# Performance work log

Measured on AMD Instinct MI355X. Metric: run time of the kernel, lower is better.

The kernel has to match this reference:

```python
import jax, jax.numpy as jnp
import numpy as np

BINS = jnp.array([1, 2, 3, 4, 8, 16, 32, 64], dtype=jnp.int32)
L = 10      # max span width
HID = 150   # Score hidden dim


def _mlp(x, W1, b1, W2, b2, W3, b3):
    # Score module: Linear -> ReLU -> Linear -> ReLU -> Linear (dropout = identity at eval)
    h = jax.nn.relu(x @ W1 + b1)
    h = jax.nn.relu(h @ W2 + b2)
    return h @ W3 + b3


def setup_inputs() -> dict:
    key = jax.random.key(0)
    ks = jax.random.split(key, 16)
    T, A, E, D, S = 8192, 1024, 512, 20, 32768
    GI = 2 * A + E + D  # 2580
    sc = lambda n: 1.0 / np.sqrt(n)
    return {
        "states": jax.random.normal(ks[0], (T, A), jnp.float32),
        "embeds": jax.random.normal(ks[1], (T, E), jnp.float32),
        "span_starts": jnp.sort(jax.random.randint(ks[2], (S,), 0, T - L)),
        "span_lengths": jax.random.randint(ks[3], (S,), 0, L),
        # attention Score params (attn_dim -> 150 -> 150 -> 1)
        "Wa1": jax.random.normal(ks[4], (A, HID), jnp.float32) * sc(A),
        "ba1": jnp.zeros((HID,), jnp.float32),
        "Wa2": jax.random.normal(ks[5], (HID, HID), jnp.float32) * sc(HID),
        "ba2": jnp.zeros((HID,), jnp.float32),
        "Wa3": jax.random.normal(ks[6], (HID, 1), jnp.float32) * sc(HID),
        "ba3": jnp.zeros((1,), jnp.float32),
        # Distance embedding table (len(bins)+1 = 9 buckets)
        "width_table": jax.random.normal(ks[7], (9, D), jnp.float32) * 0.1,
        # mention Score params (gi_dim -> 150 -> 150 -> 1)
        "Ws1": jax.random.normal(ks[8], (GI, HID), jnp.float32) * sc(GI),
        "bs1": jnp.zeros((HID,), jnp.float32),
        "Ws2": jax.random.normal(ks[9], (HID, HID), jnp.float32) * sc(HID),
        "bs2": jnp.zeros((HID,), jnp.float32),
        "Ws3": jax.random.normal(ks[10], (HID, 1), jnp.float32) * sc(HID),
        "bs3": jnp.zeros((1,), jnp.float32),
    }


def reference(states, embeds, span_starts, span_lengths,
              Wa1, ba1, Wa2, ba2, Wa3, ba3,
              width_table,
              Ws1, bs1, Ws2, bs2, Ws3, bs3):
    T = states.shape[0]
    # per-token attention logits: [T, 1]
    attns = _mlp(states, Wa1, ba1, Wa2, ba2, Wa3, ba3)

    pos = jnp.arange(L)
    idx = span_starts[:, None] + pos[None, :]                 # [S, L]
    mask = pos[None, :] <= span_lengths[:, None]              # valid positions
    idx = jnp.minimum(idx, T - 1)

    span_attn = jnp.where(mask, attns[idx, 0], -jnp.inf)      # [S, L]
    w = jax.nn.softmax(span_attn, axis=1)                     # per-span softmax
    pooled = jnp.einsum('sl,sle->se', w, embeds[idx])         # [S, E]

    ends = span_starts + span_lengths
    widths = span_lengths + 1
    bucket = jnp.searchsorted(BINS, widths.astype(jnp.int32), side='right')
    size_emb = width_table[bucket]                            # [S, D]

    g = jnp.concatenate([states[span_starts], states[ends], pooled, size_emb], axis=-1)
    scores = _mlp(g, Ws1, bs1, Ws2, bs2, Ws3, bs3)[:, 0]      # [S]
    return scores
```

## Files before the change

### kernel.cpp

```cpp
#include <hip/hip_runtime.h>
#include <math.h>

#define T_TOK 8192
#define A_DIM 1024
#define E_DIM 512
#define S_SPAN 32768
#define HID 150

typedef __attribute__((ext_vector_type(8))) short short8;
typedef __attribute__((ext_vector_type(4))) float f32x4;
typedef __attribute__((ext_vector_type(4))) unsigned int u32x4;

__device__ __forceinline__ unsigned short f2bf(float f) {
    unsigned int u = __builtin_bit_cast(unsigned int, f);
    u += 0x7FFFu + ((u >> 16) & 1u);
    return (unsigned short)(u >> 16);
}
__device__ __forceinline__ float bf2f(unsigned int h16) {
    unsigned int u = h16 << 16;
    return __builtin_bit_cast(float, u);
}
__device__ __forceinline__ short8 cast8(f32x4 a, f32x4 b) {
    short8 r;
    r[0] = (short)f2bf(a.x); r[1] = (short)f2bf(a.y);
    r[2] = (short)f2bf(a.z); r[3] = (short)f2bf(a.w);
    r[4] = (short)f2bf(b.x); r[5] = (short)f2bf(b.y);
    r[6] = (short)f2bf(b.z); r[7] = (short)f2bf(b.w);
    return r;
}

__device__ __forceinline__ void pub_barrier() {
    __builtin_amdgcn_sched_barrier(0);
    asm volatile("s_waitcnt lgkmcnt(0)" ::: "memory");
    __builtin_amdgcn_sched_barrier(0);
    __builtin_amdgcn_s_barrier();
    __builtin_amdgcn_sched_barrier(0);
}

struct WConv { const float* src; unsigned short* dst; int K0; int Kpad; int nblk; };
struct PrepTab {
    WConv g[6];
    const float* wt; const float* Ws1w; const float* bs1; float* PW;
};

__global__ __launch_bounds__(256) void prep_kernel(PrepTab tab) {
    __shared__ float tl[64][65];
    int b = blockIdx.x;
    #pragma unroll
    for (int gi = 0; gi < 6; ++gi) {
        if (b < tab.g[gi].nblk) {
            const int kt   = tab.g[gi].Kpad >> 6;
            const int j0   = (b / kt) * 64;
            const int k0   = (b % kt) * 64;
            const int K0   = tab.g[gi].K0;
            const int Kpad = tab.g[gi].Kpad;
            const int ty = threadIdx.x >> 6, tx = threadIdx.x & 63;
            const float* src = tab.g[gi].src;
            #pragma unroll
            for (int r = 0; r < 16; ++r) {
                int k = k0 + ty * 16 + r;
                int j = j0 + tx;
                tl[ty * 16 + r][tx] = (j < HID && k < K0)
                                      ? src[(size_t)k * HID + j] : 0.f;
            }
            __syncthreads();
            unsigned short* dst = tab.g[gi].dst;
            #pragma unroll
            for (int r = 0; r < 16; ++r) {
                int j = j0 + ty * 16 + r;
                if (j < 160)
                    dst[(size_t)j * Kpad + k0 + tx] = f2bf(tl[tx][ty * 16 + r]);
            }
            return;
        }
        b -= tab.g[gi].nblk;
    }
    int j = threadIdx.x;
    if (j < 160) {
        float acc = 0.f;
        if (j < HID) {
            for (int k = 0; k < 20; ++k)
                acc = fmaf(tab.wt[b * 20 + k], tab.Ws1w[k * HID + j], acc);
            acc += tab.bs1[j];
        }
        tab.PW[b * 160 + j] = acc;
    }
}

struct GG {
    const void* A; int lda;
    const unsigned short* W; int K; int nrb;
    unsigned short* outh; int ldo;
    const float* bias; int relu;
    const float* dotv; const float* dotb; float* dotout;
    const unsigned short* W2; const float* bias2;
};
struct GTab { GG g[4]; int ng; };

template <int TAG, bool AF32>
__global__ __launch_bounds__(256) void gemm_fused(GTab tab) {
    constexpr int LDW = 72;
    __shared__ unsigned short WtL[2][160 * LDW];

    int b = blockIdx.x;
    int gi = 0;
    while (gi < tab.ng - 1 && b >= tab.g[gi].nrb) { b -= tab.g[gi].nrb; ++gi; }
    const GG G = tab.g[gi];

    const int tid = threadIdx.x;
    const int wid = tid >> 6;
    const int lane = tid & 63;
    const int l15 = lane & 15;
    const int quad = lane >> 4;
    const int row0 = b * 64 + wid * 16 + l15;
    const int K = G.K;
    const int nch = K >> 6;
    const float* Af = (const float*)G.A + (size_t)row0 * G.lda;
    const unsigned short* Ah = (const unsigned short*)G.A + (size_t)row0 * G.lda;

    int sn[5], sk[5];
    #pragma unroll
    for (int i = 0; i < 5; ++i) { int u = tid + i * 256; sn[i] = u >> 3; sk[i] = (u & 7) * 8; }

    f32x4 acc[10];
    #pragma unroll
    for (int nt = 0; nt < 10; ++nt) acc[nt] = (f32x4){0.f, 0.f, 0.f, 0.f};

    u32x4 wA[5], wB[5];
    f32x4 fAa[4], fAb[4];
    short8 hAa[2], hAb[2];
    short8 avc0, avc1;

#define LOAD_W(SET, KOFF)                                                     \
    {   _Pragma("unroll")                                                     \
        for (int i = 0; i < 5; ++i)                                           \
            SET[i] = *(const u32x4*)(G.W + (size_t)sn[i] * K + (KOFF) + sk[i]); }
#define LOAD_A(FSET, HSET, KOFF)                                              \
    if (AF32) {                                                               \
        FSET[0] = *(const f32x4*)(Af + (KOFF) + quad * 8);                    \
        FSET[1] = *(const f32x4*)(Af + (KOFF) + quad * 8 + 4);                \
        FSET[2] = *(const f32x4*)(Af + (KOFF) + 32 + quad * 8);               \
        FSET[3] = *(const f32x4*)(Af + (KOFF) + 32 + quad * 8 + 4);           \
    } else {                                                                  \
        HSET[0] = *(const short8*)(Ah + (KOFF) + quad * 8);                   \
        HSET[1] = *(const short8*)(Ah + (KOFF) + 32 + quad * 8);              \
    }
#define STORE_W(SET, BUF)                                                     \
    {   _Pragma("unroll")                                                     \
        for (int i = 0; i < 5; ++i)                                           \
            *(u32x4*)&WtL[BUF][sn[i] * LDW + sk[i]] = SET[i]; }
#define SET_AVC(FSET, HSET)                                                   \
    if (AF32) { avc0 = cast8(FSET[0], FSET[1]); avc1 = cast8(FSET[2], FSET[3]); } \
    else      { avc0 = HSET[0]; avc1 = HSET[1]; }
#define MFMA_BLOCK(BUF)                                                       \
    {   _Pragma("unroll")                                                     \
        for (int nt = 0; nt < 10; ++nt) {                                     \
            short8 bv0 = *(const short8*)&WtL[BUF][(nt * 16 + l15) * LDW + quad * 8]; \
            acc[nt] = __builtin_amdgcn_mfma_f32_16x16x32_bf16(avc0, bv0, acc[nt], 0, 0, 0); \
            short8 bv1 = *(const short8*)&WtL[BUF][(nt * 16 + l15) * LDW + 32 + quad * 8]; \
            acc[nt] = __builtin_amdgcn_mfma_f32_16x16x32_bf16(avc1, bv1, acc[nt], 0, 0, 0); \
        } }

    LOAD_W(wA, 0);
    LOAD_A(fAa, hAa, 0);
    LOAD_W(wB, 64);
    LOAD_A(fAb, hAb, 64);
    STORE_W(wA, 0);
    SET_AVC(fAa, hAa);
    pub_barrier();

    for (int c = 0; c + 1 < nch; c += 2) {
        const bool mA = (c + 2 < nch);
        if (mA) {
            const int kn = (c + 2) << 6;
            LOAD_W(wA, kn);
            LOAD_A(fAa, hAa, kn);
        }
        STORE_W(wB, 1);
        MFMA_BLOCK(0);
        SET_AVC(fAb, hAb);
        pub_barrier();

        const bool mB = (c + 3 < nch);
        if (mB) {
            const int kn = (c + 3) << 6;
            LOAD_W(wB, kn);
            LOAD_A(fAb, hAb, kn);
        }
        if (mA) STORE_W(wA, 0);
        MFMA_BLOCK(1);
        if (mA) SET_AVC(fAa, hAa);
        pub_barrier();
    }
    if (nch & 1) {
        MFMA_BLOCK(0);
    }

#undef LOAD_W
#undef LOAD_A
#undef STORE_W
#undef SET_AVC
#undef MFMA_BLOCK

    const int rbase = b * 64 + wid * 16 + quad * 4;
    if (G.W2) {
        constexpr int LDH = 168;
        unsigned short* tile = &WtL[0][0] + wid * 16 * LDH;
        #pragma unroll
        for (int nt = 0; nt < 10; ++nt) {
            int col = nt * 16 + l15;
            float bv_ = (col < HID) ? G.bias[col] : 0.f;
            #pragma unroll
            for (int r = 0; r < 4; ++r) {
                float v = fmaxf(acc[nt][r] + bv_, 0.f);
                tile[(quad * 4 + r) * LDH + col] = f2bf(v);
            }
        }
        f32x4 acc2[10];
        #pragma unroll
        for (int nt = 0; nt < 10; ++nt) acc2[nt] = (f32x4){0.f, 0.f, 0.f, 0.f};
        #pragma unroll
        for (int kc = 0; kc < 5; ++kc) {
            short8 av = *(const short8*)&tile[l15 * LDH + kc * 32 + quad * 8];
            #pragma unroll
            for (int nt = 0; nt < 10; ++nt) {
                short8 bv = *(const short8*)(G.W2 + (size_t)(nt * 16 + l15) * 192 + kc * 32 + quad * 8);
                acc2[nt] = __builtin_amdgcn_mfma_f32_16x16x32_bf16(av, bv, acc2[nt], 0, 0, 0);
            }
        }
        float part[4] = {0.f, 0.f, 0.f, 0.f};
        #pragma unroll
        for (int nt = 0; nt < 10; ++nt) {
            int col = nt * 16 + l15;
            float b2 = (col < HID) ? G.bias2[col] : 0.f;
            float vv = (col < HID) ? G.dotv[col] : 0.f;
            #pragma unroll
            for (int r = 0; r < 4; ++r)
                part[r] += fmaxf(acc2[nt][r] + b2, 0.f) * vv;
        }
        #pragma unroll
        for (int r = 0; r < 4; ++r) {
            float p = part[r];
            #pragma unroll
            for (int off = 1; off < 16; off <<= 1) p += __shfl_xor(p, off);
            if (l15 == 0) G.dotout[rbase + r] = p + G.dotb[0];
        }
    } else if (G.dotout) {
        float part[4] = {0.f, 0.f, 0.f, 0.f};
        #pragma unroll
        for (int nt = 0; nt < 10; ++nt) {
            int col = nt * 16 + l15;
            float bv_ = (col < HID) ? G.bias[col] : 0.f;
            float vv = (col < HID) ? G.dotv[col] : 0.f;
            #pragma unroll
            for (int r = 0; r < 4; ++r)
                part[r] += fmaxf(acc[nt][r] + bv_, 0.f) * vv;
        }
        #pragma unroll
        for (int r = 0; r < 4; ++r) {
            float p = part[r];
            #pragma unroll
            for (int off = 1; off < 16; off <<= 1) p += __shfl_xor(p, off);
            if (l15 == 0) G.dotout[rbase + r] = p + G.dotb[0];
        }
    } else {
        #pragma unroll
        for (int nt = 0; nt < 10; ++nt) {
            int col = nt * 16 + l15;
            float bv_ = (G.bias != nullptr && col < HID) ? G.bias[col] : 0.f;
            #pragma unroll
            for (int r = 0; r < 4; ++r) {
                int row = rbase + r;
                float v = acc[nt][r] + bv_;
                if (G.relu) v = fmaxf(v, 0.f);
                G.outh[(size_t)row * G.ldo + col] = f2bf(v);
            }
        }
    }
}

__global__ __launch_bounds__(256) void span_l1_kernel(const float* __restrict__ attns,
                                                      const int* __restrict__ starts,
                                                      const int* __restrict__ lens,
                                                      const unsigned short* __restrict__ Ps,
                                                      const unsigned short* __restrict__ Pe,
                                                      const unsigned short* __restrict__ Pm,
                                                      const float* __restrict__ PW,
                                                      unsigned short* __restrict__ SH1) {
    const int wid = threadIdx.x >> 6;
    const int lane = threadIdx.x & 63;
    const int grp = lane >> 4;
    const int hl = lane & 15;
    const int gbase = lane & 48;
    const int s = blockIdx.x * 16 + wid * 4 + grp;
    const int start = starts[s];
    const int len = lens[s];

    const int iv = min(start + hl, T_TOK - 1);
    float a = (hl <= len) ? attns[iv] : -INFINITY;
    float m = a;
    #pragma unroll
    for (int off = 8; off; off >>= 1) m = fmaxf(m, __shfl_xor(m, off));
    float e = (hl <= len) ? __expf(a - m) : 0.f;
    float ssum = e;
    #pragma unroll
    for (int off = 8; off; off >>= 1) ssum += __shfl_xor(ssum, off);
    float wv = e / ssum;

    float wl[10]; int il[10];
    #pragma unroll
    for (int l = 0; l < 10; ++l) {
        wl[l] = __shfl(wv, gbase + l);
        il[l] = __shfl(iv, gbase + l);
    }

    const int end = start + len;
    const int width = len + 1;
    const int bucket = (width >= 1) + (width >= 2) + (width >= 3) + (width >= 4) +
                       (width >= 8) + (width >= 16) + (width >= 32) + (width >= 64);

    const unsigned short* ps = Ps + (size_t)start * 160;
    const unsigned short* pe = Pe + (size_t)end * 160;
    const float* pw = PW + bucket * 160;

    for (int p = hl; p < 75; p += 16) {
        const int j = 2 * p;
        unsigned int u0 = *(const unsigned int*)(ps + j);
        unsigned int u1 = *(const unsigned int*)(pe + j);
        float a0 = pw[j]     + bf2f(u0 & 0xffff) + bf2f(u1 & 0xffff);
        float a1 = pw[j + 1] + bf2f(u0 >> 16)    + bf2f(u1 >> 16);
        #pragma unroll
        for (int l = 0; l < 10; ++l) {
            unsigned int um = *(const unsigned int*)(Pm + (size_t)il[l] * 160 + j);
            a0 = fmaf(wl[l], bf2f(um & 0xffff), a0);
            a1 = fmaf(wl[l], bf2f(um >> 16), a1);
        }
        unsigned int packed = (unsigned int)f2bf(fmaxf(a0, 0.f)) |
                              ((unsigned int)f2bf(fmaxf(a1, 0.f)) << 16);
        *(unsigned int*)(SH1 + (size_t)s * 192 + j) = packed;
    }
}

extern "C" void kernel_launch(void* const* d_in, const int* in_sizes, int n_in,
                              void* d_out, int out_size, void* d_ws, size_t ws_size,
                              hipStream_t stream) {
    const float* states = (const float*)d_in[0];
    const float* embeds = (const float*)d_in[1];
    const int* span_starts = (const int*)d_in[2];
    const int* span_lengths = (const int*)d_in[3];
    const float* Wa1 = (const float*)d_in[4];
    const float* ba1 = (const float*)d_in[5];
    const float* Wa2 = (const float*)d_in[6];
    const float* ba2 = (const float*)d_in[7];
    const float* Wa3 = (const float*)d_in[8];
    const float* ba3 = (const float*)d_in[9];
    const float* width_table = (const float*)d_in[10];
    const float* Ws1 = (const float*)d_in[11];
    const float* bs1 = (const float*)d_in[12];
    const float* Ws2 = (const float*)d_in[13];
    const float* bs2 = (const float*)d_in[14];
    const float* Ws3 = (const float*)d_in[15];
    const float* bs3 = (const float*)d_in[16];
    float* out = (float*)d_out;

    char* w = (char*)d_ws;
    unsigned short* WtA  = (unsigned short*)w;  w += 480 * 1024 * 2;
    unsigned short* WtE  = (unsigned short*)w;  w += 160 * 512 * 2;
    unsigned short* Wa2t = (unsigned short*)w;  w += 160 * 192 * 2;
    unsigned short* Ws2t = (unsigned short*)w;  w += 160 * 192 * 2;
    float* PW    = (float*)w;                   w += 9 * 160 * 4;
    float* attns = (float*)w;                   w += 8192 * 4;
    unsigned short* Psh = (unsigned short*)w;   w += (size_t)T_TOK * 160 * 2;
    unsigned short* Peh = (unsigned short*)w;   w += (size_t)T_TOK * 160 * 2;
    unsigned short* Pmh = (unsigned short*)w;   w += (size_t)T_TOK * 160 * 2;
    unsigned short* SH1 = (unsigned short*)w;   w += (size_t)S_SPAN * 192 * 2;

    PrepTab pt;
    pt.g[0] = { Wa1,              WtA,              1024, 1024, 3 * (1024/64) };
    pt.g[1] = { Ws1,              WtA + 160*1024,   1024, 1024, 3 * (1024/64) };
    pt.g[2] = { Ws1 + 1024*150,   WtA + 320*1024,   1024, 1024, 3 * (1024/64) };
    pt.g[3] = { Ws1 + 2048*150,   WtE,               512,  512, 3 * (512/64)  };
    pt.g[4] = { Wa2,              Wa2t,              150,  192, 3 * (192/64)  };
    pt.g[5] = { Ws2,              Ws2t,              150,  192, 3 * (192/64)  };
    pt.wt = width_table; pt.Ws1w = Ws1 + 2560*150; pt.bs1 = bs1; pt.PW = PW;
    int wblk = 0; for (int i = 0; i < 6; ++i) wblk += pt.g[i].nblk;
    prep_kernel<<<wblk + 9, 256, 0, stream>>>(pt);

    GG z = {};

    GTab t1; t1.ng = 4;
    t1.g[0] = z; t1.g[0].A = states; t1.g[0].lda = 1024; t1.g[0].W = WtA;            t1.g[0].K = 1024;
    t1.g[0].nrb = 128; t1.g[0].bias = ba1;
    t1.g[0].W2 = Wa2t; t1.g[0].bias2 = ba2;
    t1.g[0].dotv = Wa3; t1.g[0].dotb = ba3; t1.g[0].dotout = attns;
    t1.g[1] = z; t1.g[1].A = states; t1.g[1].lda = 1024; t1.g[1].W = WtA + 160*1024; t1.g[1].K = 1024;
    t1.g[1].nrb = 128; t1.g[1].outh = Psh; t1.g[1].ldo = 160;
    t1.g[2] = z; t1.g[2].A = states; t1.g[2].lda = 1024; t1.g[2].W = WtA + 320*1024; t1.g[2].K = 1024;
    t1.g[2].nrb = 128; t1.g[2].outh = Peh; t1.g[2].ldo = 160;
    t1.g[3] = z; t1.g[3].A = embeds; t1.g[3].lda = 512;  t1.g[3].W = WtE;            t1.g[3].K = 512;
    t1.g[3].nrb = 128; t1.g[3].outh = Pmh; t1.g[3].ldo = 160;
    gemm_fused<1, true><<<512, 256, 0, stream>>>(t1);

    span_l1_kernel<<<S_SPAN / 16, 256, 0, stream>>>(attns, span_starts, span_lengths,
                                                    Psh, Peh, Pmh, PW, SH1);

    GTab t3; t3.ng = 1;
    t3.g[0] = z; t3.g[0].A = SH1; t3.g[0].lda = 192; t3.g[0].W = Ws2t; t3.g[0].K = 192;
    t3.g[0].nrb = 512; t3.g[0].bias = bs2; t3.g[0].dotv = Ws3; t3.g[0].dotb = bs3; t3.g[0].dotout = out;
    gemm_fused<3, false><<<512, 256, 0, stream>>>(t3);
}
```

Measured before the change: 166.0 us.

## Read GEMM weights directly from global memory and vectorize span layer-1 gathers

The fused GEMM drops its double-buffered LDS staging of weight tiles and its barriers. Each wave now loads bf16 weight fragments straight from global/L2 for every MFMA, and LDS is kept only for the per-wave epilogue tile. Separately, the span layer-1 kernel switches from 4-byte to 16-byte vector loads and stores, with each lane handling 8 hidden columns and the gathered row offsets premultiplied. This removes LDS traffic and synchronisation, but every wave now redundantly refetches the same weight tile from cache and loses the prefetch overlap.

```diff
diff --git a/kernel.cpp b/kernel.cpp
--- a/kernel.cpp
+++ b/kernel.cpp
@@ -27,14 +27,6 @@
     r[4] = (short)f2bf(b.x); r[5] = (short)f2bf(b.y);
     r[6] = (short)f2bf(b.z); r[7] = (short)f2bf(b.w);
     return r;
-}
-
-__device__ __forceinline__ void pub_barrier() {
-    __builtin_amdgcn_sched_barrier(0);
-    asm volatile("s_waitcnt lgkmcnt(0)" ::: "memory");
-    __builtin_amdgcn_sched_barrier(0);
-    __builtin_amdgcn_s_barrier();
-    __builtin_amdgcn_sched_barrier(0);
 }
 
 struct WConv { const float* src; unsigned short* dst; int K0; int Kpad; int nblk; };
@@ -99,8 +91,8 @@
 
 template <int TAG, bool AF32>
 __global__ __launch_bounds__(256) void gemm_fused(GTab tab) {
-    constexpr int LDW = 72;
-    __shared__ unsigned short WtL[2][160 * LDW];
+    constexpr int LDH = 168;
+    __shared__ unsigned short tileAll[4][16 * LDH];
 
     int b = blockIdx.x;
     int gi = 0;
@@ -117,95 +109,38 @@
     const int nch = K >> 6;
     const float* Af = (const float*)G.A + (size_t)row0 * G.lda;
     const unsigned short* Ah = (const unsigned short*)G.A + (size_t)row0 * G.lda;
-
-    int sn[5], sk[5];
-    #pragma unroll
-    for (int i = 0; i < 5; ++i) { int u = tid + i * 256; sn[i] = u >> 3; sk[i] = (u & 7) * 8; }
+    const unsigned short* Wr = G.W + (size_t)l15 * K;
 
     f32x4 acc[10];
     #pragma unroll
     for (int nt = 0; nt < 10; ++nt) acc[nt] = (f32x4){0.f, 0.f, 0.f, 0.f};
 
-    u32x4 wA[5], wB[5];
-    f32x4 fAa[4], fAb[4];
-    short8 hAa[2], hAb[2];
-    short8 avc0, avc1;
-
-#define LOAD_W(SET, KOFF)                                                     \
-    {   _Pragma("unroll")                                                     \
-        for (int i = 0; i < 5; ++i)                                           \
-            SET[i] = *(const u32x4*)(G.W + (size_t)sn[i] * K + (KOFF) + sk[i]); }
-#define LOAD_A(FSET, HSET, KOFF)                                              \
-    if (AF32) {                                                               \
-        FSET[0] = *(const f32x4*)(Af + (KOFF) + quad * 8);                    \
-        FSET[1] = *(const f32x4*)(Af + (KOFF) + quad * 8 + 4);                \
-        FSET[2] = *(const f32x4*)(Af + (KOFF) + 32 + quad * 8);               \
-        FSET[3] = *(const f32x4*)(Af + (KOFF) + 32 + quad * 8 + 4);           \
-    } else {                                                                  \
-        HSET[0] = *(const short8*)(Ah + (KOFF) + quad * 8);                   \
-        HSET[1] = *(const short8*)(Ah + (KOFF) + 32 + quad * 8);              \
-    }
-#define STORE_W(SET, BUF)                                                     \
-    {   _Pragma("unroll")                                                     \
-        for (int i = 0; i < 5; ++i)                                           \
-            *(u32x4*)&WtL[BUF][sn[i] * LDW + sk[i]] = SET[i]; }
-#define SET_AVC(FSET, HSET)                                                   \
-    if (AF32) { avc0 = cast8(FSET[0], FSET[1]); avc1 = cast8(FSET[2], FSET[3]); } \
-    else      { avc0 = HSET[0]; avc1 = HSET[1]; }
-#define MFMA_BLOCK(BUF)                                                       \
-    {   _Pragma("unroll")                                                     \
-        for (int nt = 0; nt < 10; ++nt) {                                     \
-            short8 bv0 = *(const short8*)&WtL[BUF][(nt * 16 + l15) * LDW + quad * 8]; \
-            acc[nt] = __builtin_amdgcn_mfma_f32_16x16x32_bf16(avc0, bv0, acc[nt], 0, 0, 0); \
-            short8 bv1 = *(const short8*)&WtL[BUF][(nt * 16 + l15) * LDW + 32 + quad * 8]; \
-            acc[nt] = __builtin_amdgcn_mfma_f32_16x16x32_bf16(avc1, bv1, acc[nt], 0, 0, 0); \
-        } }
-
-    LOAD_W(wA, 0);
-    LOAD_A(fAa, hAa, 0);
-    LOAD_W(wB, 64);
-    LOAD_A(fAb, hAb, 64);
-    STORE_W(wA, 0);
-    SET_AVC(fAa, hAa);
-    pub_barrier();
-
-    for (int c = 0; c + 1 < nch; c += 2) {
-        const bool mA = (c + 2 < nch);
-        if (mA) {
-            const int kn = (c + 2) << 6;
-            LOAD_W(wA, kn);
-            LOAD_A(fAa, hAa, kn);
-        }
-        STORE_W(wB, 1);
-        MFMA_BLOCK(0);
-        SET_AVC(fAb, hAb);
-        pub_barrier();
-
-        const bool mB = (c + 3 < nch);
-        if (mB) {
-            const int kn = (c + 3) << 6;
-            LOAD_W(wB, kn);
-            LOAD_A(fAb, hAb, kn);
-        }
-        if (mA) STORE_W(wA, 0);
-        MFMA_BLOCK(1);
-        if (mA) SET_AVC(fAa, hAa);
-        pub_barrier();
-    }
-    if (nch & 1) {
-        MFMA_BLOCK(0);
-    }
-
-#undef LOAD_W
-#undef LOAD_A
-#undef STORE_W
-#undef SET_AVC
-#undef MFMA_BLOCK
+    for (int c = 0; c < nch; ++c) {
+        const int kb = c << 6;
+        short8 avc0, avc1;
+        if (AF32) {
+            f32x4 f0 = *(const f32x4*)(Af + kb + quad * 8);
+            f32x4 f1 = *(const f32x4*)(Af + kb + quad * 8 + 4);
+            f32x4 f2 = *(const f32x4*)(Af + kb + 32 + quad * 8);
+            f32x4 f3 = *(const f32x4*)(Af + kb + 32 + quad * 8 + 4);
+            avc0 = cast8(f0, f1);
+            avc1 = cast8(f2, f3);
+        } else {
+            avc0 = *(const short8*)(Ah + kb + quad * 8);
+            avc1 = *(const short8*)(Ah + kb + 32 + quad * 8);
+        }
+        #pragma unroll
+        for (int nt = 0; nt < 10; ++nt) {
+            short8 bv0 = *(const short8*)(Wr + (size_t)nt * 16 * K + kb + quad * 8);
+            acc[nt] = __builtin_amdgcn_mfma_f32_16x16x32_bf16(avc0, bv0, acc[nt], 0, 0, 0);
+            short8 bv1 = *(const short8*)(Wr + (size_t)nt * 16 * K + kb + 32 + quad * 8);
+            acc[nt] = __builtin_amdgcn_mfma_f32_16x16x32_bf16(avc1, bv1, acc[nt], 0, 0, 0);
+        }
+    }
 
     const int rbase = b * 64 + wid * 16 + quad * 4;
     if (G.W2) {
-        constexpr int LDH = 168;
-        unsigned short* tile = &WtL[0][0] + wid * 16 * LDH;
+        unsigned short* tile = tileAll[wid];
         #pragma unroll
         for (int nt = 0; nt < 10; ++nt) {
             int col = nt * 16 + l15;
@@ -277,6 +212,19 @@
             }
         }
     }
+}
+
+__device__ __forceinline__ void add_bf8(f32x4& A, f32x4& B, u32x4 u) {
+    A.x += bf2f(u.x & 0xffff); A.y += bf2f(u.x >> 16);
+    A.z += bf2f(u.y & 0xffff); A.w += bf2f(u.y >> 16);
+    B.x += bf2f(u.z & 0xffff); B.y += bf2f(u.z >> 16);
+    B.z += bf2f(u.w & 0xffff); B.w += bf2f(u.w >> 16);
+}
+__device__ __forceinline__ void fma_bf8(f32x4& A, f32x4& B, u32x4 u, float w) {
+    A.x = fmaf(w, bf2f(u.x & 0xffff), A.x); A.y = fmaf(w, bf2f(u.x >> 16), A.y);
+    A.z = fmaf(w, bf2f(u.y & 0xffff), A.z); A.w = fmaf(w, bf2f(u.y >> 16), A.w);
+    B.x = fmaf(w, bf2f(u.z & 0xffff), B.x); B.y = fmaf(w, bf2f(u.z >> 16), B.y);
+    B.z = fmaf(w, bf2f(u.w & 0xffff), B.z); B.w = fmaf(w, bf2f(u.w >> 16), B.w);
 }
 
 __global__ __launch_bounds__(256) void span_l1_kernel(const float* __restrict__ attns,
@@ -311,7 +259,7 @@
     #pragma unroll
     for (int l = 0; l < 10; ++l) {
         wl[l] = __shfl(wv, gbase + l);
-        il[l] = __shfl(iv, gbase + l);
+        il[l] = __shfl(iv, gbase + l) * 160;
     }
 
     const int end = start + len;
@@ -323,21 +271,25 @@
     const unsigned short* pe = Pe + (size_t)end * 160;
     const float* pw = PW + bucket * 160;
 
-    for (int p = hl; p < 75; p += 16) {
-        const int j = 2 * p;
-        unsigned int u0 = *(const unsigned int*)(ps + j);
-        unsigned int u1 = *(const unsigned int*)(pe + j);
-        float a0 = pw[j]     + bf2f(u0 & 0xffff) + bf2f(u1 & 0xffff);
-        float a1 = pw[j + 1] + bf2f(u0 >> 16)    + bf2f(u1 >> 16);
-        #pragma unroll
-        for (int l = 0; l < 10; ++l) {
-            unsigned int um = *(const unsigned int*)(Pm + (size_t)il[l] * 160 + j);
-            a0 = fmaf(wl[l], bf2f(um & 0xffff), a0);
-            a1 = fmaf(wl[l], bf2f(um >> 16), a1);
-        }
-        unsigned int packed = (unsigned int)f2bf(fmaxf(a0, 0.f)) |
-                              ((unsigned int)f2bf(fmaxf(a1, 0.f)) << 16);
-        *(unsigned int*)(SH1 + (size_t)s * 192 + j) = packed;
+    #pragma unroll
+    for (int rep = 0; rep < 2; ++rep) {
+        const int c = rep * 16 + hl;
+        if (c < 20) {
+            const int j0 = c * 8;
+            f32x4 a0 = *(const f32x4*)(pw + j0);
+            f32x4 a1 = *(const f32x4*)(pw + j0 + 4);
+            add_bf8(a0, a1, *(const u32x4*)(ps + j0));
+            add_bf8(a0, a1, *(const u32x4*)(pe + j0));
+            #pragma unroll
+            for (int l = 0; l < 10; ++l)
+                fma_bf8(a0, a1, *(const u32x4*)(Pm + il[l] + j0), wl[l]);
+            u32x4 pk;
+            pk.x = (unsigned)f2bf(fmaxf(a0.x, 0.f)) | ((unsigned)f2bf(fmaxf(a0.y, 0.f)) << 16);
+            pk.y = (unsigned)f2bf(fmaxf(a0.z, 0.f)) | ((unsigned)f2bf(fmaxf(a0.w, 0.f)) << 16);
+            pk.z = (unsigned)f2bf(fmaxf(a1.x, 0.f)) | ((unsigned)f2bf(fmaxf(a1.y, 0.f)) << 16);
+            pk.w = (unsigned)f2bf(fmaxf(a1.z, 0.f)) | ((unsigned)f2bf(fmaxf(a1.w, 0.f)) << 16);
+            *(u32x4*)(SH1 + (size_t)s * 192 + j0) = pk;
+        }
     }
 }
 
```

Measured after the change: 257.2 us. +54.9%, slower.

## Pre-cast states and embeds to bf16 in prep kernel; vectorize span gather

Applied to the files above, without the earlier changes.

Adds a pass in the prep kernel that converts the fp32 states and embeds to bf16 buffers once, so the fused GEMM reads bf16 A operands and no longer reads fp32 and converts in its inner loop. Before, states was read in fp32 three times, once by each of the three GEMM groups that use it. The span layer-1 kernel is also rewritten to use 16-byte vector loads and stores over 8 columns per lane instead of 4-byte pairs. The trade-off is an extra full pass over states and embeds in the prep kernel plus a larger workspace.

```diff
diff --git a/kernel.cpp b/kernel.cpp
--- a/kernel.cpp
+++ b/kernel.cpp
@@ -41,6 +41,8 @@
 struct PrepTab {
     WConv g[6];
     const float* wt; const float* Ws1w; const float* bs1; float* PW;
+    const float* castS; unsigned short* castSd;
+    const float* castE; unsigned short* castEd;
 };
 
 __global__ __launch_bounds__(256) void prep_kernel(PrepTab tab) {
@@ -75,16 +77,28 @@
         }
         b -= tab.g[gi].nblk;
     }
-    int j = threadIdx.x;
-    if (j < 160) {
-        float acc = 0.f;
-        if (j < HID) {
-            for (int k = 0; k < 20; ++k)
-                acc = fmaf(tab.wt[b * 20 + k], tab.Ws1w[k * HID + j], acc);
-            acc += tab.bs1[j];
-        }
-        tab.PW[b * 160 + j] = acc;
-    }
+    if (b < 9) {
+        int j = threadIdx.x;
+        if (j < 160) {
+            float acc = 0.f;
+            if (j < HID) {
+                for (int k = 0; k < 20; ++k)
+                    acc = fmaf(tab.wt[b * 20 + k], tab.Ws1w[k * HID + j], acc);
+                acc += tab.bs1[j];
+            }
+            tab.PW[b * 160 + j] = acc;
+        }
+        return;
+    }
+    b -= 9;
+    const float* src; unsigned short* dst;
+    size_t base;
+    if (b < 4096) { src = tab.castS; dst = tab.castSd; base = (size_t)b * 2048; }
+    else          { src = tab.castE; dst = tab.castEd; base = (size_t)(b - 4096) * 2048; }
+    const size_t i = base + (size_t)threadIdx.x * 8;
+    f32x4 f0 = *(const f32x4*)(src + i);
+    f32x4 f1 = *(const f32x4*)(src + i + 4);
+    *(short8*)(dst + i) = cast8(f0, f1);
 }
 
 struct GG {
@@ -97,7 +111,7 @@
 };
 struct GTab { GG g[4]; int ng; };
 
-template <int TAG, bool AF32>
+template <int TAG>
 __global__ __launch_bounds__(256) void gemm_fused(GTab tab) {
     constexpr int LDW = 72;
     __shared__ unsigned short WtL[2][160 * LDW];
@@ -115,7 +129,6 @@
     const int row0 = b * 64 + wid * 16 + l15;
     const int K = G.K;
     const int nch = K >> 6;
-    const float* Af = (const float*)G.A + (size_t)row0 * G.lda;
     const unsigned short* Ah = (const unsigned short*)G.A + (size_t)row0 * G.lda;
 
     int sn[5], sk[5];
@@ -127,7 +140,6 @@
     for (int nt = 0; nt < 10; ++nt) acc[nt] = (f32x4){0.f, 0.f, 0.f, 0.f};
 
     u32x4 wA[5], wB[5];
-    f32x4 fAa[4], fAb[4];
     short8 hAa[2], hAb[2];
     short8 avc0, avc1;
 
@@ -135,23 +147,15 @@
     {   _Pragma("unroll")                                                     \
         for (int i = 0; i < 5; ++i)                                           \
             SET[i] = *(const u32x4*)(G.W + (size_t)sn[i] * K + (KOFF) + sk[i]); }
-#define LOAD_A(FSET, HSET, KOFF)                                              \
-    if (AF32) {                                                               \
-        FSET[0] = *(const f32x4*)(Af + (KOFF) + quad * 8);                    \
-        FSET[1] = *(const f32x4*)(Af + (KOFF) + quad * 8 + 4);                \
-        FSET[2] = *(const f32x4*)(Af + (KOFF) + 32 + quad * 8);               \
-        FSET[3] = *(const f32x4*)(Af + (KOFF) + 32 + quad * 8 + 4);           \
-    } else {                                                                  \
-        HSET[0] = *(const short8*)(Ah + (KOFF) + quad * 8);                   \
-        HSET[1] = *(const short8*)(Ah + (KOFF) + 32 + quad * 8);              \
-    }
+#define LOAD_A(HSET, KOFF)                                                    \
+    {   HSET[0] = *(const short8*)(Ah + (KOFF) + quad * 8);                   \
+        HSET[1] = *(const short8*)(Ah + (KOFF) + 32 + quad * 8); }
 #define STORE_W(SET, BUF)                                                     \
     {   _Pragma("unroll")                                                     \
         for (int i = 0; i < 5; ++i)                                           \
             *(u32x4*)&WtL[BUF][sn[i] * LDW + sk[i]] = SET[i]; }
-#define SET_AVC(FSET, HSET)                                                   \
-    if (AF32) { avc0 = cast8(FSET[0], FSET[1]); avc1 = cast8(FSET[2], FSET[3]); } \
-    else      { avc0 = HSET[0]; avc1 = HSET[1]; }
+#define SET_AVC(HSET)                                                         \
+    {   avc0 = HSET[0]; avc1 = HSET[1]; }
 #define MFMA_BLOCK(BUF)                                                       \
     {   _Pragma("unroll")                                                     \
         for (int nt = 0; nt < 10; ++nt) {                                     \
@@ -162,11 +166,11 @@
         } }
 
     LOAD_W(wA, 0);
-    LOAD_A(fAa, hAa, 0);
+    LOAD_A(hAa, 0);
     LOAD_W(wB, 64);
-    LOAD_A(fAb, hAb, 64);
+    LOAD_A(hAb, 64);
     STORE_W(wA, 0);
-    SET_AVC(fAa, hAa);
+    SET_AVC(hAa);
     pub_barrier();
 
     for (int c = 0; c + 1 < nch; c += 2) {
@@ -174,22 +178,22 @@
         if (mA) {
             const int kn = (c + 2) << 6;
             LOAD_W(wA, kn);
-            LOAD_A(fAa, hAa, kn);
+            LOAD_A(hAa, kn);
         }
         STORE_W(wB, 1);
         MFMA_BLOCK(0);
-        SET_AVC(fAb, hAb);
+        SET_AVC(hAb);
         pub_barrier();
 
         const bool mB = (c + 3 < nch);
         if (mB) {
             const int kn = (c + 3) << 6;
             LOAD_W(wB, kn);
-            LOAD_A(fAb, hAb, kn);
+            LOAD_A(hAb, kn);
         }
         if (mA) STORE_W(wA, 0);
         MFMA_BLOCK(1);
-        if (mA) SET_AVC(fAa, hAa);
+        if (mA) SET_AVC(hAa);
         pub_barrier();
     }
     if (nch & 1) {
@@ -277,6 +281,19 @@
             }
         }
     }
+}
+
+__device__ __forceinline__ void add_bf8(f32x4& A, f32x4& B, u32x4 u) {
+    A.x += bf2f(u.x & 0xffff); A.y += bf2f(u.x >> 16);
+    A.z += bf2f(u.y & 0xffff); A.w += bf2f(u.y >> 16);
+    B.x += bf2f(u.z & 0xffff); B.y += bf2f(u.z >> 16);
+    B.z += bf2f(u.w & 0xffff); B.w += bf2f(u.w >> 16);
+}
+__device__ __forceinline__ void fma_bf8(f32x4& A, f32x4& B, u32x4 u, float w) {
+    A.x = fmaf(w, bf2f(u.x & 0xffff), A.x); A.y = fmaf(w, bf2f(u.x >> 16), A.y);
+    A.z = fmaf(w, bf2f(u.y & 0xffff), A.z); A.w = fmaf(w, bf2f(u.y >> 16), A.w);
+    B.x = fmaf(w, bf2f(u.z & 0xffff), B.x); B.y = fmaf(w, bf2f(u.z >> 16), B.y);
+    B.z = fmaf(w, bf2f(u.w & 0xffff), B.z); B.w = fmaf(w, bf2f(u.w >> 16), B.w);
 }
 
 __global__ __launch_bounds__(256) void span_l1_kernel(const float* __restrict__ attns,
@@ -311,7 +328,7 @@
     #pragma unroll
     for (int l = 0; l < 10; ++l) {
         wl[l] = __shfl(wv, gbase + l);
-        il[l] = __shfl(iv, gbase + l);
+        il[l] = __shfl(iv, gbase + l) * 160;
     }
 
     const int end = start + len;
@@ -323,21 +340,25 @@
     const unsigned short* pe = Pe + (size_t)end * 160;
     const float* pw = PW + bucket * 160;
 
-    for (int p = hl; p < 75; p += 16) {
-        const int j = 2 * p;
-        unsigned int u0 = *(const unsigned int*)(ps + j);
-        unsigned int u1 = *(const unsigned int*)(pe + j);
-        float a0 = pw[j]     + bf2f(u0 & 0xffff) + bf2f(u1 & 0xffff);
-        float a1 = pw[j + 1] + bf2f(u0 >> 16)    + bf2f(u1 >> 16);
-        #pragma unroll
-        for (int l = 0; l < 10; ++l) {
-            unsigned int um = *(const unsigned int*)(Pm + (size_t)il[l] * 160 + j);
-            a0 = fmaf(wl[l], bf2f(um & 0xffff), a0);
-            a1 = fmaf(wl[l], bf2f(um >> 16), a1);
-        }
-        unsigned int packed = (unsigned int)f2bf(fmaxf(a0, 0.f)) |
-                              ((unsigned int)f2bf(fmaxf(a1, 0.f)) << 16);
-        *(unsigned int*)(SH1 + (size_t)s * 192 + j) = packed;
+    #pragma unroll
+    for (int rep = 0; rep < 2; ++rep) {
+        const int c = rep * 16 + hl;
+        if (c < 20) {
+            const int j0 = c * 8;
+            f32x4 a0 = *(const f32x4*)(pw + j0);
+            f32x4 a1 = *(const f32x4*)(pw + j0 + 4);
+            add_bf8(a0, a1, *(const u32x4*)(ps + j0));
+            add_bf8(a0, a1, *(const u32x4*)(pe + j0));
+            #pragma unroll
+            for (int l = 0; l < 10; ++l)
+                fma_bf8(a0, a1, *(const u32x4*)(Pm + il[l] + j0), wl[l]);
+            u32x4 pk;
+            pk.x = (unsigned)f2bf(fmaxf(a0.x, 0.f)) | ((unsigned)f2bf(fmaxf(a0.y, 0.f)) << 16);
+            pk.y = (unsigned)f2bf(fmaxf(a0.z, 0.f)) | ((unsigned)f2bf(fmaxf(a0.w, 0.f)) << 16);
+            pk.z = (unsigned)f2bf(fmaxf(a1.x, 0.f)) | ((unsigned)f2bf(fmaxf(a1.y, 0.f)) << 16);
+            pk.w = (unsigned)f2bf(fmaxf(a1.z, 0.f)) | ((unsigned)f2bf(fmaxf(a1.w, 0.f)) << 16);
+            *(u32x4*)(SH1 + (size_t)s * 192 + j0) = pk;
+        }
     }
 }
 
@@ -374,6 +395,8 @@
     unsigned short* Peh = (unsigned short*)w;   w += (size_t)T_TOK * 160 * 2;
     unsigned short* Pmh = (unsigned short*)w;   w += (size_t)T_TOK * 160 * 2;
     unsigned short* SH1 = (unsigned short*)w;   w += (size_t)S_SPAN * 192 * 2;
+    unsigned short* SB  = (unsigned short*)w;   w += (size_t)T_TOK * A_DIM * 2;
+    unsigned short* EB  = (unsigned short*)w;   w += (size_t)T_TOK * E_DIM * 2;
 
     PrepTab pt;
     pt.g[0] = { Wa1,              WtA,              1024, 1024, 3 * (1024/64) };
@@ -383,23 +406,25 @@
     pt.g[4] = { Wa2,              Wa2t,              150,  192, 3 * (192/64)  };
     pt.g[5] = { Ws2,              Ws2t,              150,  192, 3 * (192/64)  };
     pt.wt = width_table; pt.Ws1w = Ws1 + 2560*150; pt.bs1 = bs1; pt.PW = PW;
+    pt.castS = states; pt.castSd = SB;
+    pt.castE = embeds; pt.castEd = EB;
     int wblk = 0; for (int i = 0; i < 6; ++i) wblk += pt.g[i].nblk;
-    prep_kernel<<<wblk + 9, 256, 0, stream>>>(pt);
+    prep_kernel<<<wblk + 9 + 4096 + 2048, 256, 0, stream>>>(pt);
 
     GG z = {};
 
     GTab t1; t1.ng = 4;
-    t1.g[0] = z; t1.g[0].A = states; t1.g[0].lda = 1024; t1.g[0].W = WtA;            t1.g[0].K = 1024;
+    t1.g[0] = z; t1.g[0].A = SB; t1.g[0].lda = 1024; t1.g[0].W = WtA;            t1.g[0].K = 1024;
     t1.g[0].nrb = 128; t1.g[0].bias = ba1;
     t1.g[0].W2 = Wa2t; t1.g[0].bias2 = ba2;
     t1.g[0].dotv = Wa3; t1.g[0].dotb = ba3; t1.g[0].dotout = attns;
-    t1.g[1] = z; t1.g[1].A = states; t1.g[1].lda = 1024; t1.g[1].W = WtA + 160*1024; t1.g[1].K = 1024;
+    t1.g[1] = z; t1.g[1].A = SB; t1.g[1].lda = 1024; t1.g[1].W = WtA + 160*1024; t1.g[1].K = 1024;
     t1.g[1].nrb = 128; t1.g[1].outh = Psh; t1.g[1].ldo = 160;
-    t1.g[2] = z; t1.g[2].A = states; t1.g[2].lda = 1024; t1.g[2].W = WtA + 320*1024; t1.g[2].K = 1024;
+    t1.g[2] = z; t1.g[2].A = SB; t1.g[2].lda = 1024; t1.g[2].W = WtA + 320*1024; t1.g[2].K = 1024;
     t1.g[2].nrb = 128; t1.g[2].outh = Peh; t1.g[2].ldo = 160;
-    t1.g[3] = z; t1.g[3].A = embeds; t1.g[3].lda = 512;  t1.g[3].W = WtE;            t1.g[3].K = 512;
+    t1.g[3] = z; t1.g[3].A = EB; t1.g[3].lda = 512;  t1.g[3].W = WtE;            t1.g[3].K = 512;
     t1.g[3].nrb = 128; t1.g[3].outh = Pmh; t1.g[3].ldo = 160;
-    gemm_fused<1, true><<<512, 256, 0, stream>>>(t1);
+    gemm_fused<1><<<512, 256, 0, stream>>>(t1);
 
     span_l1_kernel<<<S_SPAN / 16, 256, 0, stream>>>(attns, span_starts, span_lengths,
                                                     Psh, Peh, Pmh, PW, SH1);
@@ -407,5 +432,5 @@
     GTab t3; t3.ng = 1;
     t3.g[0] = z; t3.g[0].A = SH1; t3.g[0].lda = 192; t3.g[0].W = Ws2t; t3.g[0].K = 192;
     t3.g[0].nrb = 512; t3.g[0].bias = bs2; t3.g[0].dotv = Ws3; t3.g[0].dotb = bs3; t3.g[0].dotout = out;
-    gemm_fused<3, false><<<512, 256, 0, stream>>>(t3);
-}
+    gemm_fused<3><<<512, 256, 0, stream>>>(t3);
+}
```

Result: no change. 166.9 us (+0.5%).
